# Kernel tuning notes

Measured on AMD Instinct MI355X. Metric: run time of the kernel, lower is better.

Reference implementation:

```python
import jax, jax.numpy as jnp
import numpy as np

B, IN, T, E, S, K, W, HD = 4096, 512, 10, 16, 2, 4, 1024, 64


def setup_inputs() -> dict:
    key = jax.random.key(0)
    ks = jax.random.split(key, 12)
    he = lambda k, shp, fan: jax.random.normal(k, shp, jnp.float32) * (2.0 / fan) ** 0.5
    x = jax.random.normal(ks[0], (B, IN + T), jnp.float32)
    return {
        'x': x,
        'gk': he(ks[1], (T, E), T),
        'rk0': he(ks[2], (E, IN, W), IN),
        'rb0': jax.random.normal(ks[3], (E, W), jnp.float32) * 0.01,
        'rk1': he(ks[4], (E, W, W), W),
        'rb1': jax.random.normal(ks[5], (E, W), jnp.float32) * 0.01,
        'sk0': he(ks[6], (S, IN, W), IN),
        'sb0': jax.random.normal(ks[7], (S, W), jnp.float32) * 0.01,
        'sk1': he(ks[8], (S, W, W), W),
        'sb1': jax.random.normal(ks[9], (S, W), jnp.float32) * 0.01,
        'hk': he(ks[10], (T, W, HD), W),
        'hb': jax.random.normal(ks[11], (T, HD), jnp.float32) * 0.01,
    }


def reference(x, gk, rk0, rb0, rk1, rb1, sk0, sb0, sk1, sb1, hk, hb):
    task_idx = x[:, -T:]            # (B, T) task one-hot / features
    feat = x[:, :-T]                # (B, IN)

    # --- top-k routing on task features ---
    gating_logits = task_idx @ gk                       # (B, E)
    topk_idx = jnp.argsort(-gating_logits, axis=-1)[:, :K]  # (B, K)
    topk_logits = jnp.take_along_axis(gating_logits, topk_idx, axis=-1)
    topk_weights = jax.nn.softmax(topk_logits, axis=-1)     # (B, K)

    # --- routed experts: run every expert chain densely, gather at the end ---
    # h: (B, E, d); each expert's independent MLP chain over the same input.
    h = jnp.broadcast_to(feat[:, None, :], (B, E, IN))
    h = jax.nn.relu(jnp.einsum('bei,eij->bej', h, rk0) + rb0[None])  # (B, E, W)
    h = jax.nn.relu(jnp.einsum('bei,eij->bej', h, rk1) + rb1[None])  # (B, E, W)
    h_sel = jnp.take_along_axis(h, topk_idx[:, :, None], axis=1)     # (B, K, W)
    routed = jnp.einsum('bkw,bk->bw', h_sel, topk_weights)           # (B, W)

    # --- shared experts: all run, mean-combined ---
    hs = jnp.broadcast_to(feat[:, None, :], (B, S, IN))
    hs = jax.nn.relu(jnp.einsum('bsi,sij->bsj', hs, sk0) + sb0[None])
    hs = jax.nn.relu(jnp.einsum('bsi,sij->bsj', hs, sk1) + sb1[None])
    shared = hs.mean(axis=1)                                         # (B, W)

    features_out = jnp.tanh(routed + shared)                         # (B, W)

    # --- per-task heads, select by task id ---
    heads_out = jnp.einsum('bw,twd->btd', features_out, hk) + hb[None]  # (B, T, HD)
    task_indices = task_idx.argmax(axis=-1)                             # (B,)
    out = jnp.take_along_axis(heads_out, task_indices[:, None, None], axis=1)[:, 0]
    return out
```

## Files before the change

### kernel.cpp

```cpp
#include <hip/hip_runtime.h>

typedef unsigned short u16;
typedef __attribute__((ext_vector_type(8))) short bf16x8;
typedef __attribute__((ext_vector_type(4))) float f32x4;

constexpr int B_ = 4096, IN_ = 512, T_ = 10, E_ = 16, S_ = 2, K_ = 4, W_ = 1024, HD_ = 64;
constexpr int XROW = IN_ + T_;
constexpr int NPAIR = B_ * (K_ + S_);
constexpr int MTU = 208;
constexpr int GEMM_GRID = MTU * 8;
constexpr int GB_ = 16;
constexpr int CB_GRID = 1034;


#define GLL16(g, l) __builtin_amdgcn_global_load_lds( \
    (const __attribute__((address_space(1))) void*)(g), \
    (__attribute__((address_space(3))) void*)(l), 16, 0, 0)

__device__ __forceinline__ u16 f2bf(float x) {
    unsigned u = __float_as_uint(x);
    return (u16)((u + 0x7fffu + ((u >> 16) & 1u)) >> 16);
}
__device__ __forceinline__ float bf2f(u16 b) { return __uint_as_float(((unsigned)b) << 16); }

__global__ __launch_bounds__(256) void featconv(const float* __restrict__ x, u16* __restrict__ featb) {
    int i = blockIdx.x * 256 + threadIdx.x;
    int b = i >> 8;
    int c2 = (i & 255) * 2;
    float2 v = *(const float2*)(x + (size_t)b * XROW + c2);
    ushort2 o;
    o.x = f2bf(v.x);
    o.y = f2bf(v.y);
    *(ushort2*)(featb + (size_t)b * IN_ + c2) = o;
}

__global__ __launch_bounds__(256) void gate_kernel(const float* __restrict__ x, const float* __restrict__ gk,
                                                   int* __restrict__ top4p, float* __restrict__ w6,
                                                   int* __restrict__ task_id, int* __restrict__ tpp,
                                                   int* __restrict__ bct_e, int* __restrict__ bct_t) {
    __shared__ float sgk[T_ * E_];
    __shared__ int hist[E_];
    __shared__ int thist[T_];
    int blk = blockIdx.x, tid = threadIdx.x;
    int b = blk * 256 + tid;
    if (tid < T_ * E_) sgk[tid] = gk[tid];
    if (tid < E_) hist[tid] = 0;
    if (tid < T_) thist[tid] = 0;
    __syncthreads();
    float tv[T_];
#pragma unroll
    for (int i = 0; i < T_; ++i) tv[i] = x[(size_t)b * XROW + IN_ + i];
    float lg[E_];
#pragma unroll
    for (int e = 0; e < E_; ++e) {
        float s = 0.f;
#pragma unroll
        for (int i = 0; i < T_; ++i) s += tv[i] * sgk[i * E_ + e];
        lg[e] = s;
    }
    int idx[K_]; float val[K_];
#pragma unroll
    for (int k = 0; k < K_; ++k) {
        int bi = 0; float bv = -1e30f;
#pragma unroll
        for (int e = 0; e < E_; ++e)
            if (lg[e] > bv) { bv = lg[e]; bi = e; }
        idx[k] = bi; val[k] = bv; lg[bi] = -1e30f;
    }
    float m = val[0];
    float ex[K_]; float s = 0.f;
#pragma unroll
    for (int k = 0; k < K_; ++k) { ex[k] = expf(val[k] - m); s += ex[k]; }
    float inv = 1.f / s;
#pragma unroll
    for (int k = 0; k < K_; ++k) {
        int lp = atomicAdd(&hist[idx[k]], 1);
        top4p[b * K_ + k] = idx[k] | (lp << 8);
        w6[b * 6 + k] = ex[k] * inv;
    }
    w6[b * 6 + 4] = 0.5f;
    w6[b * 6 + 5] = 0.5f;
    int ti = 0; float tb = tv[0];
#pragma unroll
    for (int i = 1; i < T_; ++i)
        if (tv[i] > tb) { tb = tv[i]; ti = i; }
    task_id[b] = ti;
    tpp[b] = atomicAdd(&thist[ti], 1);
    __syncthreads();
    if (tid < E_) bct_e[blk * E_ + tid] = hist[tid];
    if (tid < T_) bct_t[blk * T_ + tid] = thist[tid];
}

__global__ void build_tables(const int* __restrict__ bct_e, const int* __restrict__ bct_t,
                             int* __restrict__ meta, int* __restrict__ blockbase,
                             int* __restrict__ tblockbase) {
    __shared__ int cnt_s[E_], tcnt_s[T_], base_s[E_], pb_s[T_];
    int tid = threadIdx.x;
    if (tid < E_) {
        int s = 0;
        for (int blk = 0; blk < GB_; ++blk) s += bct_e[blk * E_ + tid];
        cnt_s[tid] = s;
        meta[tid] = s;
    }
    if (tid >= 32 && tid < 32 + T_) {
        int t = tid - 32;
        int s = 0;
        for (int blk = 0; blk < GB_; ++blk) s += bct_t[blk * T_ + t];
        tcnt_s[t] = s;
        meta[91 + t] = s;
    }
    __syncthreads();
    if (tid == 0) {
        int a = 0;
        for (int e = 0; e < E_; ++e) { base_s[e] = a; meta[16 + e] = a; a += cnt_s[e]; }
        int t = 0;
        for (int g = 0; g < 18; ++g) { meta[48 + g] = t; int c = (g < 16) ? cnt_s[g] : B_; t += (c + 127) >> 7; }
        meta[66] = t;
        int pr = 0, br = 0;
        for (int i = 0; i < T_; ++i) {
            pb_s[i] = pr;
            meta[70 + i] = pr;
            meta[80 + i] = br;
            pr += ((tcnt_s[i] + 3) >> 2) << 2;
            br += (tcnt_s[i] + 3) >> 2;
        }
        meta[90] = br;
    }
    __syncthreads();
    if (tid < E_) {
        int run = base_s[tid];
        for (int blk = 0; blk < GB_; ++blk) { blockbase[blk * E_ + tid] = run; run += bct_e[blk * E_ + tid]; }
    }
    if (tid >= 32 && tid < 32 + T_) {
        int t = tid - 32;
        int run = pb_s[t];
        for (int blk = 0; blk < GB_; ++blk) { tblockbase[blk * T_ + t] = run; run += bct_t[blk * T_ + t]; }
    }
}

__global__ __launch_bounds__(256) void scatter_kernel(const int* __restrict__ top4p,
                                                      const int* __restrict__ blockbase,
                                                      const int* __restrict__ task_id, const int* __restrict__ tpp,
                                                      const int* __restrict__ tblockbase,
                                                      int* __restrict__ pair_sample, int* __restrict__ pair_dst,
                                                      int* __restrict__ torder) {
    int blk = blockIdx.x, tid = threadIdx.x;
    int b = blk * 256 + tid;
#pragma unroll
    for (int k = 0; k < K_; ++k) {
        int v = top4p[b * K_ + k];
        int e = v & 0xFF, lp = v >> 8;
        int p = blockbase[blk * E_ + e] + lp;
        pair_sample[p] = b;
        pair_dst[p] = b * 6 + k;
    }
    pair_sample[B_ * K_ + b] = b;       pair_dst[B_ * K_ + b] = b * 6 + 4;
    pair_sample[B_ * K_ + B_ + b] = b;  pair_dst[B_ * K_ + B_ + b] = b * 6 + 5;
    torder[tblockbase[blk * T_ + task_id[b]] + tpp[b]] = b;
}

__global__ __launch_bounds__(256) void convbf16(const float* __restrict__ in, u16* __restrict__ out) {
    int i = blockIdx.x * 256 + threadIdx.x;
    float4 v = ((const float4*)in)[i];
    ushort4 o;
    o.x = f2bf(v.x); o.y = f2bf(v.y); o.z = f2bf(v.z); o.w = f2bf(v.w);
    ((ushort4*)out)[i] = o;
}

__global__ __launch_bounds__(256) void transconv2(const float* __restrict__ srcA, const float* __restrict__ srcB,
                                                  int splitZ, u16* __restrict__ out, int K, int N) {
    __shared__ float tile[32][33];
    int z = blockIdx.z;
    const float* src = (z < splitZ) ? (srcA + (size_t)z * K * N) : (srcB + (size_t)(z - splitZ) * K * N);
    int k0 = blockIdx.y * 32, n0 = blockIdx.x * 32;
    int tid = threadIdx.x;
    int r = tid >> 3, c4 = (tid & 7) * 4;
    float4 v = *(const float4*)(src + (size_t)(k0 + r) * N + n0 + c4);
    tile[r][c4 + 0] = v.x; tile[r][c4 + 1] = v.y; tile[r][c4 + 2] = v.z; tile[r][c4 + 3] = v.w;
    __syncthreads();
    ushort4 ov;
    ov.x = f2bf(tile[c4 + 0][r]);
    ov.y = f2bf(tile[c4 + 1][r]);
    ov.z = f2bf(tile[c4 + 2][r]);
    ov.w = f2bf(tile[c4 + 3][r]);
    *(ushort4*)(out + (size_t)z * N * K + (size_t)(n0 + r) * K + k0 + c4) = ov;
}

template <int K, int LAYER>
__global__ __launch_bounds__(256, 4) void gemm6(const u16* __restrict__ Asrc, const u16* __restrict__ wT,
                                                const float* __restrict__ rbias, const float* __restrict__ sbias,
                                                const int* __restrict__ pair_sample, const int* __restrict__ pair_dst,
                                                const int* __restrict__ meta, u16* __restrict__ outp) {
    __shared__ char lds[32768];
    const int* tpre = meta + 48;
    const int nwg = tpre[18] * 8;
    int p = blockIdx.x;
    if (p >= nwg) return;
    int q = nwg >> 3, r8 = nwg & 7;
    int xcd = p & 7, iofs = p >> 3;
    int lid = (xcd < r8 ? xcd * (q + 1) : r8 * (q + 1) + (xcd - r8) * q) + iofs;
    int mtu = lid >> 3, nt = lid & 7;
    int e = 0;
    while (mtu >= tpre[e + 1]) ++e;
    int mt = mtu - tpre[e];
    int off, cnt;
    if (e < E_) { off = meta[16 + e]; cnt = meta[e]; }
    else        { off = B_ * K_ + (e - E_) * B_; cnt = B_; }

    const int tid = threadIdx.x;
    const int srow = tid >> 2, sslot = tid & 3;
    const u16* wTe = wT + (size_t)e * W_ * K;
    const u16* ab[2];
    const u16* bb[2];
#pragma unroll
    for (int r = 0; r < 2; ++r) {
        int row = r * 64 + srow;
        int gchunk = sslot ^ ((row >> 1) & 3);
        int gm = mt * 128 + row;
        if (gm >= cnt) gm = cnt - 1;
        int arow = (LAYER == 1) ? pair_sample[off + gm] : (off + gm);
        ab[r] = Asrc + (size_t)arow * K + gchunk * 8;
        bb[r] = wTe + (size_t)(nt * 128 + row) * K + gchunk * 8;
    }

    auto STAGE = [&](int kt, int buf) {
        char* base = lds + buf * 16384;
        GLL16(ab[0] + kt * 32, base + tid * 16);
        GLL16(ab[1] + kt * 32, base + 4096 + tid * 16);
        GLL16(bb[0] + kt * 32, base + 8192 + tid * 16);
        GLL16(bb[1] + kt * 32, base + 12288 + tid * 16);
    };

    f32x4 acc[4][4];
#pragma unroll
    for (int i = 0; i < 4; ++i)
#pragma unroll
        for (int j = 0; j < 4; ++j) acc[i][j] = (f32x4){0.f, 0.f, 0.f, 0.f};

    const int lane = tid & 63, wid = tid >> 6;
    const int wr = wid >> 1, wc = wid & 1;
    const int fr = lane & 15;
    const int fkb = (lane >> 4) * 16;

    constexpr int NKT = K / 32;
    STAGE(0, 0);
    asm volatile("s_waitcnt vmcnt(0)" ::: "memory");
    __builtin_amdgcn_s_barrier();
    asm volatile("" ::: "memory");
    int cur = 0;
    for (int kt = 0; kt < NKT; ++kt) {
        if (kt + 1 < NKT) STAGE(kt + 1, cur ^ 1);
        char* A = lds + cur * 16384;
        char* Bv = A + 8192;
        bf16x8 af[4], bf[4];
#pragma unroll
        for (int i = 0; i < 4; ++i) {
            int arow = wr * 64 + i * 16 + fr;
            af[i] = *(const bf16x8*)(A + arow * 64 + (fkb ^ (((arow >> 1) & 3) << 4)));
            int brow = wc * 64 + i * 16 + fr;
            bf[i] = *(const bf16x8*)(Bv + brow * 64 + (fkb ^ (((brow >> 1) & 3) << 4)));
        }
#pragma unroll
        for (int i = 0; i < 4; ++i)
#pragma unroll
            for (int j = 0; j < 4; ++j)
                acc[i][j] = __builtin_amdgcn_mfma_f32_16x16x32_bf16(af[i], bf[j], acc[i][j], 0, 0, 0);
        asm volatile("s_waitcnt vmcnt(0)" ::: "memory");
        __builtin_amdgcn_s_barrier();
        asm volatile("" ::: "memory");
        cur ^= 1;
    }

    const float* bias = (e < E_) ? (rbias + (size_t)e * W_) : (sbias + (size_t)(e - E_) * W_);
#pragma unroll
    for (int i = 0; i < 4; ++i) {
#pragma unroll
        for (int reg = 0; reg < 4; ++reg) {
            int r = wr * 64 + i * 16 + (lane >> 4) * 4 + reg;
#pragma unroll
            for (int j = 0; j < 4; ++j) {
                int c = wc * 64 + j * 16 + fr;
                float v = acc[i][j][reg] + bias[nt * 128 + c];
                *(u16*)(lds + r * 256 + ((c * 2) ^ ((r & 7) << 4))) = f2bf(fmaxf(v, 0.f));
            }
        }
    }
    __syncthreads();
#pragma unroll
    for (int rr = 0; rr < 8; ++rr) {
        int flat = rr * 4096 + tid * 16;
        int r = flat >> 8;
        int co = flat & 255;
        int m = mt * 128 + r;
        if (m < cnt) {
            int outrow = (LAYER == 1) ? (off + m) : pair_dst[off + m];
            bf16x8 v = *(const bf16x8*)(lds + r * 256 + (co ^ ((r & 7) << 4)));
            *(bf16x8*)(outp + (size_t)outrow * W_ + nt * 128 + (co >> 1)) = v;
        }
    }
}

__global__ __launch_bounds__(256) void combine4(const u16* __restrict__ h2, const float* __restrict__ w6,
                                                const int* __restrict__ torder, const int* __restrict__ meta,
                                                const u16* __restrict__ hkb, const float* __restrict__ hb,
                                                float* __restrict__ out) {
    __shared__ float f[4][W_];
    __shared__ float partials[4][4][64];
    const int* bp = meta + 80;
    int blk = blockIdx.x;
    if (blk >= bp[T_]) return;
    int t = 0;
    while (blk >= bp[t + 1]) ++t;
    int slot0 = meta[70 + t] + (blk - bp[t]) * 4;
    int vend  = meta[70 + t] + meta[91 + t];
    int tid = threadIdx.x;
    int s0 = torder[slot0];
    int smp[4];
#pragma unroll
    for (int i = 0; i < 4; ++i) {
        int v = torder[slot0 + i];
        smp[i] = (slot0 + i < vend) ? v : s0;
    }
#pragma unroll
    for (int s = 0; s < 4; ++s) {
        int b = smp[s];
        float wsl[6];
#pragma unroll
        for (int qq = 0; qq < 6; ++qq) wsl[qq] = w6[b * 6 + qq];
        float sum[4] = {0.f, 0.f, 0.f, 0.f};
#pragma unroll
        for (int qq = 0; qq < 6; ++qq) {
            ushort4 v = *(const ushort4*)(h2 + (size_t)(b * 6 + qq) * W_ + tid * 4);
            sum[0] += wsl[qq] * bf2f(v.x);
            sum[1] += wsl[qq] * bf2f(v.y);
            sum[2] += wsl[qq] * bf2f(v.z);
            sum[3] += wsl[qq] * bf2f(v.w);
        }
#pragma unroll
        for (int i = 0; i < 4; ++i) f[s][tid * 4 + i] = tanhf(sum[i]);
    }
    __syncthreads();
    int d = tid & 63, g = tid >> 6;
    const u16* hp = hkb + (size_t)t * W_ * HD_ + d;
    float acc[4] = {0.f, 0.f, 0.f, 0.f};
#pragma unroll 4
    for (int w = g; w < W_; w += 4) {
        float hv = bf2f(hp[(size_t)w * HD_]);
#pragma unroll
        for (int s = 0; s < 4; ++s) acc[s] += f[s][w] * hv;
    }
#pragma unroll
    for (int s = 0; s < 4; ++s) partials[g][s][d] = acc[s];
    __syncthreads();
    int ss = tid >> 6, dd = tid & 63;
    float r = partials[0][ss][dd] + partials[1][ss][dd] + partials[2][ss][dd] + partials[3][ss][dd]
            + hb[t * HD_ + dd];
    out[(size_t)smp[ss] * HD_ + dd] = r;
}

extern "C" void kernel_launch(void* const* d_in, const int* in_sizes, int n_in,
                              void* d_out, int out_size, void* d_ws, size_t ws_size,
                              hipStream_t stream) {
    const float* x   = (const float*)d_in[0];
    const float* gk  = (const float*)d_in[1];
    const float* rk0 = (const float*)d_in[2];
    const float* rb0 = (const float*)d_in[3];
    const float* rk1 = (const float*)d_in[4];
    const float* rb1 = (const float*)d_in[5];
    const float* sk0 = (const float*)d_in[6];
    const float* sb0 = (const float*)d_in[7];
    const float* sk1 = (const float*)d_in[8];
    const float* sb1 = (const float*)d_in[9];
    const float* hk  = (const float*)d_in[10];
    const float* hb  = (const float*)d_in[11];
    float* out = (float*)d_out;
    (void)in_sizes; (void)n_in; (void)out_size; (void)ws_size;

    char* ws = (char*)d_ws;
    size_t o = 0;
    auto alloc = [&](size_t bytes) { char* p = ws + o; o += (bytes + 255) & ~(size_t)255; return p; };
    int* meta        = (int*)alloc(512);
    int* bct_e       = (int*)alloc((size_t)GB_ * E_ * 4);
    int* bct_t       = (int*)alloc((size_t)GB_ * T_ * 4);
    int* blockbase   = (int*)alloc((size_t)GB_ * E_ * 4);
    int* tblockbase  = (int*)alloc((size_t)GB_ * T_ * 4);
    int* top4p       = (int*)alloc((size_t)B_ * K_ * 4);
    float* w6        = (float*)alloc((size_t)B_ * 6 * 4);
    int* task_id     = (int*)alloc((size_t)B_ * 4);
    int* tpp         = (int*)alloc((size_t)B_ * 4);
    int* pair_sample = (int*)alloc((size_t)NPAIR * 4);
    int* pair_dst    = (int*)alloc((size_t)NPAIR * 4);
    int* torder      = (int*)alloc((size_t)(B_ + 64) * 4);
    u16* featb       = (u16*)alloc((size_t)B_ * IN_ * 2);
    u16* w0T         = (u16*)alloc((size_t)(E_ + S_) * W_ * IN_ * 2);
    u16* w1T         = (u16*)alloc((size_t)(E_ + S_) * W_ * W_ * 2);
    u16* hkb         = (u16*)alloc((size_t)T_ * W_ * HD_ * 2);
    u16* h1          = (u16*)alloc((size_t)NPAIR * W_ * 2);
    u16* h2          = (u16*)alloc((size_t)NPAIR * W_ * 2);

    featconv<<<B_, 256, 0, stream>>>(x, featb);
    gate_kernel<<<GB_, 256, 0, stream>>>(x, gk, top4p, w6, task_id, tpp, bct_e, bct_t);
    build_tables<<<1, 64, 0, stream>>>(bct_e, bct_t, meta, blockbase, tblockbase);
    scatter_kernel<<<GB_, 256, 0, stream>>>(top4p, blockbase, task_id, tpp, tblockbase,
                                            pair_sample, pair_dst, torder);
    transconv2<<<dim3(W_ / 32, IN_ / 32, E_ + S_), 256, 0, stream>>>(rk0, sk0, E_, w0T, IN_, W_);
    transconv2<<<dim3(W_ / 32, W_ / 32, E_ + S_), 256, 0, stream>>>(rk1, sk1, E_, w1T, W_, W_);
    convbf16<<<(T_ * W_ * HD_) / 1024, 256, 0, stream>>>(hk, hkb);
    gemm6<IN_, 1><<<GEMM_GRID, 256, 0, stream>>>(featb, w0T, rb0, sb0, pair_sample, pair_dst, meta, h1);
    gemm6<W_, 2><<<GEMM_GRID, 256, 0, stream>>>(h1, w1T, rb1, sb1, pair_sample, pair_dst, meta, h2);
    combine4<<<CB_GRID, 256, 0, stream>>>(h2, w6, torder, meta, hkb, hb, out);
}
```

Baseline: 192.5 us.

## Triple-buffer GEMM K-loop, widen weight transpose tiles, vectorize tanh store

The grouped expert GEMMs now keep three LDS stages instead of two and prefetch two K-tiles ahead. Each iteration waits with vmcnt(4) instead of draining every outstanding load, so global-to-LDS copies overlap more of the MFMA work; to fit the larger LDS footprint the occupancy hint drops from 4 to 3 blocks per CU. The weight transpose/bf16 conversion kernel now handles 64x32 tiles with 16-byte bf16x8 stores, halving its block count. The combine kernel writes its tanh results to LDS as float4.

```diff
diff --git a/kernel.cpp b/kernel.cpp
--- a/kernel.cpp
+++ b/kernel.cpp
@@ -167,31 +167,33 @@
     ((ushort4*)out)[i] = o;
 }
 
-__global__ __launch_bounds__(256) void transconv2(const float* __restrict__ srcA, const float* __restrict__ srcB,
+__global__ __launch_bounds__(256) void transconv3(const float* __restrict__ srcA, const float* __restrict__ srcB,
                                                   int splitZ, u16* __restrict__ out, int K, int N) {
-    __shared__ float tile[32][33];
+    __shared__ float tile[64][33];
     int z = blockIdx.z;
     const float* src = (z < splitZ) ? (srcA + (size_t)z * K * N) : (srcB + (size_t)(z - splitZ) * K * N);
-    int k0 = blockIdx.y * 32, n0 = blockIdx.x * 32;
+    int k0 = blockIdx.y * 64, n0 = blockIdx.x * 32;
     int tid = threadIdx.x;
-    int r = tid >> 3, c4 = (tid & 7) * 4;
-    float4 v = *(const float4*)(src + (size_t)(k0 + r) * N + n0 + c4);
-    tile[r][c4 + 0] = v.x; tile[r][c4 + 1] = v.y; tile[r][c4 + 2] = v.z; tile[r][c4 + 3] = v.w;
-    __syncthreads();
-    ushort4 ov;
-    ov.x = f2bf(tile[c4 + 0][r]);
-    ov.y = f2bf(tile[c4 + 1][r]);
-    ov.z = f2bf(tile[c4 + 2][r]);
-    ov.w = f2bf(tile[c4 + 3][r]);
-    *(ushort4*)(out + (size_t)z * N * K + (size_t)(n0 + r) * K + k0 + c4) = ov;
+    int r = tid >> 2, c8 = (tid & 3) * 8;
+    const float* s0 = src + (size_t)(k0 + r) * N + n0 + c8;
+    float4 v0 = *(const float4*)s0;
+    float4 v1 = *(const float4*)(s0 + 4);
+    tile[r][c8 + 0] = v0.x; tile[r][c8 + 1] = v0.y; tile[r][c8 + 2] = v0.z; tile[r][c8 + 3] = v0.w;
+    tile[r][c8 + 4] = v1.x; tile[r][c8 + 5] = v1.y; tile[r][c8 + 6] = v1.z; tile[r][c8 + 7] = v1.w;
+    __syncthreads();
+    int n = tid >> 3, kc = (tid & 7) * 8;
+    u16 o[8];
+#pragma unroll
+    for (int j = 0; j < 8; ++j) o[j] = f2bf(tile[kc + j][n]);
+    *(bf16x8*)(out + (size_t)z * N * K + (size_t)(n0 + n) * K + k0 + kc) = *(const bf16x8*)o;
 }
 
 template <int K, int LAYER>
-__global__ __launch_bounds__(256, 4) void gemm6(const u16* __restrict__ Asrc, const u16* __restrict__ wT,
+__global__ __launch_bounds__(256, 3) void gemm8(const u16* __restrict__ Asrc, const u16* __restrict__ wT,
                                                 const float* __restrict__ rbias, const float* __restrict__ sbias,
                                                 const int* __restrict__ pair_sample, const int* __restrict__ pair_dst,
                                                 const int* __restrict__ meta, u16* __restrict__ outp) {
-    __shared__ char lds[32768];
+    __shared__ char lds[49152];
     const int* tpre = meta + 48;
     const int nwg = tpre[18] * 8;
     int p = blockIdx.x;
@@ -244,13 +246,19 @@
 
     constexpr int NKT = K / 32;
     STAGE(0, 0);
-    asm volatile("s_waitcnt vmcnt(0)" ::: "memory");
+    __builtin_amdgcn_sched_barrier(0);
+    STAGE(1, 1);
+    asm volatile("s_waitcnt vmcnt(4)" ::: "memory");
     __builtin_amdgcn_s_barrier();
     asm volatile("" ::: "memory");
-    int cur = 0;
+    __builtin_amdgcn_sched_barrier(0);
+    int rb = 0, sb = 2;
     for (int kt = 0; kt < NKT; ++kt) {
-        if (kt + 1 < NKT) STAGE(kt + 1, cur ^ 1);
-        char* A = lds + cur * 16384;
+        if (kt + 2 < NKT) {
+            STAGE(kt + 2, sb);
+            sb = (sb == 2) ? 0 : sb + 1;
+        }
+        char* A = lds + rb * 16384;
         char* Bv = A + 8192;
         bf16x8 af[4], bf[4];
 #pragma unroll
@@ -265,10 +273,16 @@
 #pragma unroll
             for (int j = 0; j < 4; ++j)
                 acc[i][j] = __builtin_amdgcn_mfma_f32_16x16x32_bf16(af[i], bf[j], acc[i][j], 0, 0, 0);
-        asm volatile("s_waitcnt vmcnt(0)" ::: "memory");
+        __builtin_amdgcn_sched_barrier(0);
+        if (kt + 2 < NKT) {
+            asm volatile("s_waitcnt vmcnt(4) lgkmcnt(0)" ::: "memory");
+        } else {
+            asm volatile("s_waitcnt vmcnt(0) lgkmcnt(0)" ::: "memory");
+        }
         __builtin_amdgcn_s_barrier();
         asm volatile("" ::: "memory");
-        cur ^= 1;
+        __builtin_amdgcn_sched_barrier(0);
+        rb = (rb == 2) ? 0 : rb + 1;
     }
 
     const float* bias = (e < E_) ? (rbias + (size_t)e * W_) : (sbias + (size_t)(e - E_) * W_);
@@ -336,8 +350,9 @@
             sum[2] += wsl[qq] * bf2f(v.z);
             sum[3] += wsl[qq] * bf2f(v.w);
         }
-#pragma unroll
-        for (int i = 0; i < 4; ++i) f[s][tid * 4 + i] = tanhf(sum[i]);
+        float4 tf;
+        tf.x = tanhf(sum[0]); tf.y = tanhf(sum[1]); tf.z = tanhf(sum[2]); tf.w = tanhf(sum[3]);
+        *(float4*)(&f[s][tid * 4]) = tf;
     }
     __syncthreads();
     int d = tid & 63, g = tid >> 6;
@@ -403,10 +418,10 @@
     build_tables<<<1, 64, 0, stream>>>(bct_e, bct_t, meta, blockbase, tblockbase);
     scatter_kernel<<<GB_, 256, 0, stream>>>(top4p, blockbase, task_id, tpp, tblockbase,
                                             pair_sample, pair_dst, torder);
-    transconv2<<<dim3(W_ / 32, IN_ / 32, E_ + S_), 256, 0, stream>>>(rk0, sk0, E_, w0T, IN_, W_);
-    transconv2<<<dim3(W_ / 32, W_ / 32, E_ + S_), 256, 0, stream>>>(rk1, sk1, E_, w1T, W_, W_);
+    transconv3<<<dim3(W_ / 32, IN_ / 64, E_ + S_), 256, 0, stream>>>(rk0, sk0, E_, w0T, IN_, W_);
+    transconv3<<<dim3(W_ / 32, W_ / 64, E_ + S_), 256, 0, stream>>>(rk1, sk1, E_, w1T, W_, W_);
     convbf16<<<(T_ * W_ * HD_) / 1024, 256, 0, stream>>>(hk, hkb);
-    gemm6<IN_, 1><<<GEMM_GRID, 256, 0, stream>>>(featb, w0T, rb0, sb0, pair_sample, pair_dst, meta, h1);
-    gemm6<W_, 2><<<GEMM_GRID, 256, 0, stream>>>(h1, w1T, rb1, sb1, pair_sample, pair_dst, meta, h2);
+    gemm8<IN_, 1><<<GEMM_GRID, 256, 0, stream>>>(featb, w0T, rb0, sb0, pair_sample, pair_dst, meta, h1);
+    gemm8<W_, 2><<<GEMM_GRID, 256, 0, stream>>>(h1, w1T, rb1, sb1, pair_sample, pair_dst, meta, h2);
     combine4<<<CB_GRID, 256, 0, stream>>>(h2, w6, torder, meta, hkb, hb, out);
 }
```

New measurement: 192.8 us. No clear change (+0.1%).
